# Performance work log

Hardware: AMD Instinct MI355X
Metric: run time of the kernel (lower is better)

## Reference

```python
import jax, jax.numpy as jnp
import numpy as np

S = 32   # parent grid side
G = 64   # child grid side (2*S)
C = 16   # channels
DN = ('NDHWC', 'DHWIO', 'NDHWC')


def conv3(t, w, b):
    # t: [D,H,W,Cin] dense grid; zero padding == nonexistent coords contribute 0 (ME semantics)
    return jax.lax.conv_general_dilated(t[None], w, (1, 1, 1), 'SAME', dimension_numbers=DN)[0] + b


def _grids():
    ix = jnp.arange(G)
    px = (ix % 2)[:, None, None]
    py = (ix % 2)[None, :, None]
    pz = (ix % 2)[None, None, :]
    oct_m = {(a, b, c): (px == a) & (py == b) & (pz == c)
             for a in (0, 1) for b in (0, 1) for c in (0, 1)}
    groups6 = [[(0, 0, 0)], [(1, 1, 0)], [(1, 0, 1)], [(0, 1, 1)],
               [(1, 0, 0), (0, 1, 0)], [(0, 0, 1), (1, 1, 1)]]
    g6 = [jnp.any(jnp.stack([oct_m[o] for o in g]), 0) for g in groups6]
    s3 = (ix // 2)[:, None, None] + (ix // 2)[None, :, None] + (ix // 2)[None, None, :]
    m3 = [(s3 % 3) == j for j in range(3)]  # 3-way repartition (group_mask_gen_par)
    return g6, m3


def coder(feat, occ, w1, b1, w2, b2):
    # ProbCoder: conv -> ReLU -> conv -> sigmoid; outputs exist only at input coords
    of = occ[..., None].astype(feat.dtype)
    h = jax.nn.relu(conv3(feat, w1, b1)) * of
    return jax.nn.sigmoid(conv3(h, w2, b2)) * of


def union(a, b):
    (fa, oa), (fb, ob) = a, b
    return (jnp.where(oa[..., None], fa, fb), oa | ob)


def _forward(x, w_down, b_down, w_fel1, b_fel1, w_fel2, b_fel2, w_up, b_up,
             wc1, bc1, wc2, bc2, wl1, bl1, wl2, bl2):
    g6, m3 = _grids()
    occ_x = x[..., 0] > 0                                    # GT occupied child voxels
    # down (stride-2 conv): coordinate effect only -- last_POV uses ones_like features
    p_occ = jnp.any(occ_x.reshape(S, 2, S, 2, S, 2), axis=(1, 3, 5))  # parent coords
    pf = p_occ[..., None].astype(x.dtype)                    # last_POV features (ones)
    # FEL (dfa): conv(1->C,k3)+ReLU+conv(C->C,k3), outputs only at existing parents
    h = jax.nn.relu(conv3(pf, w_fel1, b_fel1)) * pf
    h = conv3(h, w_fel2, b_fel2) * pf                        # [S,S,S,C]
    # generative transposed conv k2 s2: each parent emits 8 children (octant-specific weight)
    up = jnp.einsum('xyzc,ocd->xyzod', h, w_up) + b_up       # [S,S,S,8,C]
    up = up.reshape(S, S, S, 2, 2, 2, C).transpose(0, 3, 1, 4, 2, 5, 6).reshape(G, G, G, C)
    occ = jnp.repeat(jnp.repeat(jnp.repeat(p_occ, 2, 0), 2, 1), 2, 2)  # child coords of prob
    prob_f = up * occ[..., None]
    lab = [occ_x & g for g in g6]                            # generate_label: GT per group
    # ---------- anchor1 compression (3 sub-stages inside octant group 1) ----------
    a1_o = occ & g6[0]
    a1_f = prob_f * a1_o[..., None]
    r = [(a1_f * m[..., None], a1_o & m) for m in m3]
    lab1 = [lab[0] & m for m in m3]
    p11 = coder(r[0][0], r[0][1], wc1[0], bc1[0], wc2[0], bc2[0])
    d1s = (prob_f * lab1[0][..., None], lab1[0])             # decoded GT of sub-stage 1
    in2 = union(r[1], d1s)
    p12 = coder(in2[0], in2[1], wl1[0], bl1[0], wl2[0], bl2[0]) * (in2[1] & m3[1])[..., None]
    d2s = (prob_f * lab1[1][..., None], lab1[1])
    in3 = union(union(d1s, d2s), r[2])
    p13 = coder(in3[0], in3[1], wl1[1], bl1[1], wl2[1], bl2[1]) * (in3[1] & m3[2])[..., None]
    # ---------- anchors 2..6 ----------
    dec = (prob_f * lab[0][..., None], lab[0])               # prob_anchor1_dec
    probs = [p11, p12, p13]
    for k in range(1, 6):
        ak_o = occ & g6[k]
        ak = (prob_f * ak_o[..., None], ak_o)
        inp = union(dec, ak)
        pk = coder(inp[0], inp[1], wc1[k], bc1[k], wc2[k], bc2[k]) * (inp[1] & g6[k])[..., None]
        probs.append(pk)
        if k < 5:
            dk = (prob_f * lab[k][..., None], lab[k])
            dec = union(dec, dk)
    probs = jnp.stack([p[..., 0] for p in probs], 0)          # [8,G,G,G]
    labels = jnp.stack([lab1[0], lab1[1], lab1[2], lab[1], lab[2], lab[3], lab[4], lab[5]], 0).astype(x.dtype)
    return probs, labels


def setup_inputs() -> dict:
    key = jax.random.key(0)
    ks = jax.random.split(key, 20)
    f = lambda k, s: jax.random.normal(k, s, jnp.float32) * 0.1
    x = (jax.random.uniform(ks[0], (G, G, G, 1)) < 0.5).astype(jnp.float32)
    return {
        'x': x,
        'w_down': f(ks[1], (2, 2, 2, 1, 1)), 'b_down': f(ks[2], (1,)),
        'w_fel1': f(ks[3], (3, 3, 3, 1, C)), 'b_fel1': f(ks[4], (C,)),
        'w_fel2': f(ks[5], (3, 3, 3, C, C)), 'b_fel2': f(ks[6], (C,)),
        'w_up': f(ks[7], (8, C, C)), 'b_up': f(ks[8], (C,)),
        'wc1': f(ks[9], (6, 3, 3, 3, C, C)), 'bc1': f(ks[10], (6, C)),
        'wc2': f(ks[11], (6, 3, 3, 3, C, 1)), 'bc2': f(ks[12], (6, 1)),
        'wl1': f(ks[13], (2, 5, 5, 5, C, C)), 'bl1': f(ks[14], (2, C)),
        'wl2': f(ks[15], (2, 5, 5, 5, C, 1)), 'bl2': f(ks[16], (2, 1)),
    }


def reference(x, w_down, b_down, w_fel1, b_fel1, w_fel2, b_fel2, w_up, b_up,
              wc1, bc1, wc2, bc2, wl1, bl1, wl2, bl2):
    return _forward(x, w_down, b_down, w_fel1, b_fel1, w_fel2, b_fel2, w_up, b_up,
                    wc1, bc1, wc2, bc2, wl1, bl1, wl2, bl2)
```

## Files before the change

kernel.cpp:

```cpp
#include <hip/hip_runtime.h>
#include <cstdint>
#include <math.h>

#define G 64
#define S 32
#define G3 (G*G*G)
#define S3 (S*S*S)

typedef unsigned long long u64;
typedef unsigned int u32;
typedef unsigned short u16;

typedef __attribute__((ext_vector_type(8))) short s16x8;
typedef __attribute__((ext_vector_type(4))) float f32x4;

__device__ __forceinline__ float sigmoidf_(float v) {
    return 1.0f / (1.0f + expf(-v));
}
__device__ __forceinline__ u32 f2bf_rne(float f) {
    u32 u = __float_as_uint(f);
    u += 0x7fff + ((u >> 16) & 1);
    return u >> 16;
}
__device__ __forceinline__ u64 rfl64(u64 v) {
    u32 lo = __builtin_amdgcn_readfirstlane((u32)v);
    u32 hi = __builtin_amdgcn_readfirstlane((u32)(v >> 32));
    return ((u64)hi << 32) | lo;
}
__device__ __forceinline__ u64 tap_hit(u64 wout, u64 wn, int dz) {
    return (dz >= 0) ? (wout & (wn >> dz)) : (wout & (wn << (-dz)));
}
__device__ __forceinline__ void gload16(const void* g, void* l) {
    __builtin_amdgcn_global_load_lds(
        (const __attribute__((address_space(1))) unsigned int*)g,
        (__attribute__((address_space(3))) unsigned int*)l, 16, 0, 0);
}

__global__ __launch_bounds__(256) void k_pocc(const float* __restrict__ x,
                                              unsigned char* __restrict__ pocc) {
    int p = blockIdx.x * 256 + threadIdx.x;
    if (p >= S3) return;
    int pz = p & 31, py = (p >> 5) & 31, px = p >> 10;
    const float* b = x + (((size_t)(px * 2) * G + py * 2) * G + pz * 2);
    bool occ = false;
    #pragma unroll
    for (int a = 0; a < 2; a++)
        #pragma unroll
        for (int bb = 0; bb < 2; bb++)
            #pragma unroll
            for (int c = 0; c < 2; c++)
                occ = occ || (b[((size_t)a * G + bb) * G + c] > 0.0f);
    pocc[p] = occ ? 1 : 0;
}

__global__ __launch_bounds__(256) void k_fel1(const unsigned char* __restrict__ pocc,
                                              const float* __restrict__ w1,
                                              const float* __restrict__ b1,
                                              float* __restrict__ h1) {
    int idx = blockIdx.x * 256 + threadIdx.x;
    int p = idx >> 4, co = idx & 15;
    int pz = p & 31, py = (p >> 5) & 31, px = p >> 10;
    if (!pocc[p]) { h1[idx] = 0.0f; return; }
    float a = b1[co];
    for (int dx = -1; dx <= 1; ++dx) {
        int nx = px + dx; if ((unsigned)nx >= S) continue;
        for (int dy = -1; dy <= 1; ++dy) {
            int ny = py + dy; if ((unsigned)ny >= S) continue;
            for (int dz = -1; dz <= 1; ++dz) {
                int nz = pz + dz; if ((unsigned)nz >= S) continue;
                if (pocc[(nx * S + ny) * S + nz])
                    a += w1[(((dx + 1) * 3 + (dy + 1)) * 3 + (dz + 1)) * 16 + co];
            }
        }
    }
    h1[idx] = fmaxf(a, 0.0f);
}

__global__ __launch_bounds__(256) void k_fel2(const unsigned char* __restrict__ pocc,
                                              const float* __restrict__ h1,
                                              const float* __restrict__ w2,
                                              const float* __restrict__ b2,
                                              float* __restrict__ h2) {
    int idx = blockIdx.x * 256 + threadIdx.x;
    int p = idx >> 4, co = idx & 15;
    int pz = p & 31, py = (p >> 5) & 31, px = p >> 10;
    if (!pocc[p]) { h2[idx] = 0.0f; return; }
    float a = b2[co];
    for (int dx = -1; dx <= 1; ++dx) {
        int nx = px + dx; if ((unsigned)nx >= S) continue;
        for (int dy = -1; dy <= 1; ++dy) {
            int ny = py + dy; if ((unsigned)ny >= S) continue;
            for (int dz = -1; dz <= 1; ++dz) {
                int nz = pz + dz; if ((unsigned)nz >= S) continue;
                const float* f = h1 + (size_t)((nx * S + ny) * S + nz) * 16;
                const float* ww = w2 + (size_t)(((dx + 1) * 3 + (dy + 1)) * 3 + (dz + 1)) * 256 + co;
                #pragma unroll
                for (int ci = 0; ci < 16; ++ci)
                    a = fmaf(f[ci], ww[ci * 16], a);
            }
        }
    }
    h2[idx] = a;
}

__global__ __launch_bounds__(256) void k_up(const unsigned char* __restrict__ pocc,
                                            const float* __restrict__ h2,
                                            const float* __restrict__ wup,
                                            const float* __restrict__ bup,
                                            u16* __restrict__ pf) {
    int idx = blockIdx.x * 256 + threadIdx.x;
    int p = idx >> 3, o = idx & 7;
    int pz = p & 31, py = (p >> 5) & 31, px = p >> 10;
    bool occ = pocc[p] != 0;
    int a = o >> 2, b = (o >> 1) & 1, c = o & 1;
    int line = (2 * px + a) * G + (2 * py + b);
    u16* op = pf + ((size_t)line * 64 + (2 * pz + c)) * 16;
    uint4* o4 = reinterpret_cast<uint4*>(op);
    if (!occ) {
        o4[0] = make_uint4(0, 0, 0, 0);
        o4[1] = make_uint4(0, 0, 0, 0);
        return;
    }
    float h[16];
    const float* hp = h2 + (size_t)p * 16;
    #pragma unroll
    for (int i = 0; i < 16; i++) h[i] = hp[i];
    u32 pk[8];
    #pragma unroll
    for (int i = 0; i < 8; ++i) {
        float a0 = bup[2 * i], a1 = bup[2 * i + 1];
        #pragma unroll
        for (int cc = 0; cc < 16; cc++) {
            a0 = fmaf(h[cc], wup[(o * 16 + cc) * 16 + 2 * i], a0);
            a1 = fmaf(h[cc], wup[(o * 16 + cc) * 16 + 2 * i + 1], a1);
        }
        pk[i] = f2bf_rne(a0) | (f2bf_rne(a1) << 16);
    }
    o4[0] = make_uint4(pk[0], pk[1], pk[2], pk[3]);
    o4[1] = make_uint4(pk[4], pk[5], pk[6], pk[7]);
}

__global__ __launch_bounds__(256) void k_masks(const float* __restrict__ x,
                                               const unsigned char* __restrict__ pocc,
                                               u64* __restrict__ lw_in,
                                               u64* __restrict__ lw_fin,
                                               unsigned char* __restrict__ m_in,
                                               float* __restrict__ labels) {
    int z = threadIdx.x;
    int y = blockIdx.x * 4 + threadIdx.y;
    int xx = blockIdx.y;
    int v = (xx * G + y) * G + z;
    int par = ((xx & 1) << 2) | ((y & 1) << 1) | (z & 1);
    const int gmap[8] = {0, 5, 4, 3, 4, 2, 1, 5};
    int g = gmap[par];
    int t = ((xx >> 1) + (y >> 1) + (z >> 1)) % 3;
    bool occ = pocc[(((xx >> 1) * S) + (y >> 1)) * S + (z >> 1)] != 0;
    bool ox = x[v] > 0.0f;
    bool g0 = (g == 0);

    bool mi[8], mf[8], lb[8];
    mi[0] = occ && g0 && (t == 0);
    mi[1] = (occ && g0 && (t == 1)) || (ox && g0 && (t == 0));
    mi[2] = (ox && g0 && (t < 2)) || (occ && g0 && (t == 2));
    mi[3] = (ox && g0)       || (occ && (g == 1));
    mi[4] = (ox && (g <= 1)) || (occ && (g == 2));
    mi[5] = (ox && (g <= 2)) || (occ && (g == 3));
    mi[6] = (ox && (g <= 3)) || (occ && (g == 4));
    mi[7] = (ox && (g <= 4)) || (occ && (g == 5));

    mf[0] = occ && g0 && (t == 0);
    mf[1] = occ && g0 && (t == 1);
    mf[2] = occ && g0 && (t == 2);
    mf[3] = occ && (g == 1);
    mf[4] = occ && (g == 2);
    mf[5] = occ && (g == 3);
    mf[6] = occ && (g == 4);
    mf[7] = occ && (g == 5);

    lb[0] = ox && g0 && (t == 0);
    lb[1] = ox && g0 && (t == 1);
    lb[2] = ox && g0 && (t == 2);
    lb[3] = ox && (g == 1);
    lb[4] = ox && (g == 2);
    lb[5] = ox && (g == 3);
    lb[6] = ox && (g == 4);
    lb[7] = ox && (g == 5);

    int line = xx * G + y;
    u32 mbyte = 0;
    #pragma unroll
    for (int c = 0; c < 8; ++c) {
        u64 wi = __ballot((int)mi[c]);
        u64 wf = __ballot((int)mf[c]);
        if (z == 0) {
            lw_in[c * 4096 + line] = wi;
            lw_fin[c * 4096 + line] = wf;
        }
        mbyte |= ((u32)mi[c]) << c;
        labels[(size_t)c * G3 + v] = lb[c] ? 1.0f : 0.0f;
    }
    m_in[v] = (unsigned char)mbyte;
}

__global__ __launch_bounds__(256) void k_maskprob(const u16* __restrict__ pf,
                                                  const unsigned char* __restrict__ m_in,
                                                  u16* __restrict__ mprob,
                                                  int b0, int nb) {
    int gid = blockIdx.x * 256 + threadIdx.x;
    size_t off = (size_t)gid * 8;
    uint4 d = *reinterpret_cast<const uint4*>(pf + off);
    unsigned char mb = m_in[gid >> 1];
    const uint4 z = make_uint4(0, 0, 0, 0);
    for (int ci = 0; ci < nb; ++ci) {
        int c = b0 + ci;
        uint4 o = ((mb >> c) & 1) ? d : z;
        *reinterpret_cast<uint4*>(mprob + (size_t)ci * G3 * 16 + off) = o;
    }
}

#define FRAGSTRIDE 38400
__global__ __launch_bounds__(64) void k_prep_bfrag(const float* __restrict__ wc1,
                                                   const float* __restrict__ wl1,
                                                   u16* __restrict__ bfrag) {
    int c = blockIdx.x;
    int frag = blockIdx.y;
    int lane = threadIdx.x;
    bool is5 = (c == 1 || c == 2);
    int R = is5 ? 2 : 1;
    int KS = 2 * R + 1;
    int npair = R + 1;
    int nfrag = KS * KS * npair;
    if (frag >= nfrag) return;
    const float* W = is5 ? (wl1 + (size_t)(c - 1) * 32000)
                         : (wc1 + (size_t)((c == 0) ? 0 : (c - 2)) * 6912);
    int dxdy = frag / npair, p = frag - dxdy * npair;
    int dziA = 2 * p;
    int co = lane & 15, kg = lane >> 4;
    u16 outv[8];
    #pragma unroll
    for (int j = 0; j < 8; ++j) {
        int k = kg * 8 + j;
        int ci = k & 15;
        int dzi = (k < 16) ? dziA : (dziA + 1);
        float v = 0.0f;
        if (dzi < KS)
            v = W[(size_t)(dxdy * KS + dzi) * 256 + ci * 16 + co];
        outv[j] = (u16)f2bf_rne(v);
    }
    u16* o = bfrag + (size_t)c * FRAGSTRIDE + ((size_t)frag * 64 + lane) * 8;
    uint4 pk;
    pk.x = outv[0] | ((u32)outv[1] << 16);
    pk.y = outv[2] | ((u32)outv[3] << 16);
    pk.z = outv[4] | ((u32)outv[5] << 16);
    pk.w = outv[6] | ((u32)outv[7] << 16);
    *reinterpret_cast<uint4*>(o) = pk;
}

__global__ __launch_bounds__(256) void k_conv1_mfma(const u16* __restrict__ mprob,
                                                    const u64* __restrict__ lw_in,
                                                    const u16* __restrict__ bfrag,
                                                    const float* __restrict__ bc1,
                                                    const float* __restrict__ bl1,
                                                    u16* __restrict__ hbase,
                                                    int b0) {
    int ci = blockIdx.y;
    int c = b0 + ci;
    bool is5 = (c == 1 || c == 2);
    int R = is5 ? 2 : 1;
    int KS = 2 * R + 1, npair = R + 1;
    const u64* lw = lw_in + (size_t)c * 4096;
    u16* h_c = hbase + (size_t)ci * G3 * 16;
    const u16* mp = mprob + (size_t)ci * G3 * 16;
    const u16* bf = bfrag + (size_t)c * FRAGSTRIDE;
    const float* bptr = is5 ? (bl1 + (c - 1) * 16)
                            : (bc1 + ((c == 0) ? 0 : (c - 2)) * 16);

    int x = blockIdx.x >> 4;
    int y0 = (blockIdx.x & 15) << 2;
    int w = threadIdx.y;
    int lane = threadIdx.x;
    int yw = y0 + w;

    u64 w0 = rfl64(lw[x * G + yw]);
    u64 anyw = lw[x * G + y0] | lw[x * G + y0 + 1] | lw[x * G + y0 + 2] | lw[x * G + y0 + 3];
    if (anyw == 0ULL) return;

    __shared__ u32 lds[8 * 2304 / 4];
    char* ldsc = reinterpret_cast<char*>(lds);

    int col = lane & 15, kg = lane >> 4;
    float bv = bptr[col];
    f32x4 acc[4];
    #pragma unroll
    for (int s = 0; s < 4; ++s) acc[s] = (f32x4){bv, bv, bv, bv};

    int t = w * 64 + lane;
    if (t < 128) {
        int slot = t >> 4, q = t & 15;
        int off = (q < 8) ? (q * 16) : (2176 + (q - 8) * 16);
        *reinterpret_cast<uint4*>(ldsc + slot * 2304 + off) = make_uint4(0, 0, 0, 0);
    }

    u32 goff = ((u32)lane >> 1) * 32 +
               ((((u32)lane & 1) ^ (((u32)lane >> 3) & 1) ^ 1u) * 16);

    int nlines = 4 + 2 * R;

    for (int dx = -R; dx <= R; ++dx) {
        int nx = x + dx;
        __syncthreads();
        if ((unsigned)nx < G) {
            for (int s = w; s < nlines; s += 4) {
                int ny = y0 - R + s;
                if ((unsigned)ny >= G) continue;
                if (lw[nx * G + ny] == 0ULL) continue;
                const char* src = reinterpret_cast<const char*>(mp + (size_t)(nx * G + ny) * 1024) + goff;
                char* dst = ldsc + s * 2304 + 128;
                gload16(src, dst);
                gload16(src + 1024, dst + 1024);
            }
        }
        __syncthreads();
        if (w0 == 0ULL || (unsigned)nx >= G) continue;

        for (int dy = -R; dy <= R; ++dy) {
            int ny = yw + dy;
            if ((unsigned)ny >= G) continue;
            u64 wn = rfl64(lw[nx * G + ny]);
            if (wn == 0ULL) continue;
            int slot = w + dy + R;
            for (int p = 0; p < npair; ++p) {
                int dzA = -R + 2 * p;
                int dzB = dzA + 1;
                bool hasB = (dzB <= R);
                u64 hit = tap_hit(w0, wn, dzA);
                if (hasB) hit |= tap_hit(w0, wn, dzB);
                if (hit == 0ULL) continue;
                int frag = ((dx + R) * KS + (dy + R)) * npair + p;
                s16x8 bf8 = *reinterpret_cast<const s16x8*>(bf + ((size_t)frag * 64 + lane) * 8);
                int dz = (kg < 2) ? dzA : (hasB ? dzB : dzA);
                int lzb = col + dz + 4;
                const char* ab = ldsc + slot * 2304 + lzb * 32
                                 + (((kg & 1) ^ ((lzb >> 2) & 1)) * 16);
                #pragma unroll
                for (int s = 0; s < 4; ++s) {
                    if (((hit >> (s * 16)) & 0xFFFFULL) == 0ULL) continue;
                    s16x8 a = *reinterpret_cast<const s16x8*>(ab + s * 512);
                    acc[s] = __builtin_amdgcn_mfma_f32_16x16x32_bf16(a, bf8, acc[s], 0, 0, 0);
                }
            }
        }
    }

    if (w0 == 0ULL) return;
    u16* hline = h_c + (size_t)(x * G + yw) * G * 16;
    #pragma unroll
    for (int s = 0; s < 4; ++s) {
        #pragma unroll
        for (int r = 0; r < 4; ++r) {
            int z = s * 16 + kg * 4 + r;
            if ((w0 >> z) & 1) {
                float v = fmaxf(acc[s][r], 0.0f);
                hline[z * 16 + col] = (u16)f2bf_rne(v);
            }
        }
    }
}

template <int KS>
__device__ __forceinline__ void conv2_body(const u32* __restrict__ h_c,
                                           const u64* __restrict__ lwi,
                                           const u64* __restrict__ lwf,
                                           const float* __restrict__ w2,
                                           const float* __restrict__ b2,
                                           float* __restrict__ outp) {
    const int R = KS / 2;
    int z = threadIdx.x;
    int line = blockIdx.x * 4 + threadIdx.y;
    int xx = line >> 6, y = line & 63;
    int v = (xx * G + y) * G + z;
    u64 wf = rfl64(lwf[line]);
    if (wf == 0ULL) { outp[v] = 0.0f; return; }
    bool m = (wf >> z) & 1;

    float ac0 = 0.0f, ac1 = 0.0f;
    for (int dx = -R; dx <= R; ++dx) {
        int nx = xx + dx; if ((unsigned)nx >= G) continue;
        for (int dy = -R; dy <= R; ++dy) {
            int ny = y + dy; if ((unsigned)ny >= G) continue;
            u64 wn = rfl64(lwi[nx * G + ny]);
            if (wn == 0ULL) continue;
            const float* wbase = w2 + (size_t)(((dx + R) * KS + (dy + R)) * KS) * 16;
            #pragma unroll
            for (int dz = -R; dz <= R; ++dz) {
                if (tap_hit(wf, wn, dz) == 0ULL) continue;
                int nz = z + dz;
                bool ok = (unsigned)nz < G;
                int nzc = ok ? nz : 0;
                bool mn = ok && ((wn >> nzc) & 1);
                const float* w = wbase + (dz + R) * 16;
                if (mn) {
                    const uint4* h4 = reinterpret_cast<const uint4*>(
                        h_c + ((size_t)((nx * G + ny) * G + nzc)) * 8);
                    uint4 Ua = h4[0], Ub = h4[1];
                    u32 uu[8] = {Ua.x, Ua.y, Ua.z, Ua.w, Ub.x, Ub.y, Ub.z, Ub.w};
                    float s0 = 0.0f, s1 = 0.0f;
                    #pragma unroll
                    for (int i = 0; i < 8; ++i) {
                        float lo = __uint_as_float(uu[i] << 16);
                        float hi = __uint_as_float(uu[i] & 0xffff0000u);
                        s0 = fmaf(lo, w[2 * i], s0);
                        s1 = fmaf(hi, w[2 * i + 1], s1);
                    }
                    if (((dz + R) & 1) == 0) ac0 += s0 + s1;
                    else                     ac1 += s0 + s1;
                }
            }
        }
    }
    float acc = b2[0] + ac0 + ac1;
    outp[v] = m ? sigmoidf_(acc) : 0.0f;
}

__global__ __launch_bounds__(256) void k_conv2_all(const u32* __restrict__ hbase,
                                                   const u64* __restrict__ lw_in,
                                                   const u64* __restrict__ lw_fin,
                                                   const float* __restrict__ wc2,
                                                   const float* __restrict__ bc2,
                                                   const float* __restrict__ wl2,
                                                   const float* __restrict__ bl2,
                                                   float* __restrict__ out,
                                                   int b0) {
    int ci = blockIdx.y;
    int c = b0 + ci;
    const u64* lwi = lw_in + (size_t)c * 4096;
    const u64* lwf = lw_fin + (size_t)c * 4096;
    const u32* h_c = hbase + (size_t)ci * G3 * 8;
    float* outp = out + (size_t)c * G3;
    if (c == 1 || c == 2) {
        conv2_body<5>(h_c, lwi, lwf, wl2 + (size_t)(c - 1) * 2000, bl2 + (c - 1), outp);
    } else {
        int j = (c == 0) ? 0 : (c - 2);
        conv2_body<3>(h_c, lwi, lwf, wc2 + (size_t)j * 432, bc2 + j, outp);
    }
}

extern "C" void kernel_launch(void* const* d_in, const int* in_sizes, int n_in,
                              void* d_out, int out_size, void* d_ws, size_t ws_size,
                              hipStream_t stream) {
    const float* x      = (const float*)d_in[0];
    const float* w_fel1 = (const float*)d_in[3];
    const float* b_fel1 = (const float*)d_in[4];
    const float* w_fel2 = (const float*)d_in[5];
    const float* b_fel2 = (const float*)d_in[6];
    const float* w_up   = (const float*)d_in[7];
    const float* b_up   = (const float*)d_in[8];
    const float* wc1    = (const float*)d_in[9];
    const float* bc1    = (const float*)d_in[10];
    const float* wc2    = (const float*)d_in[11];
    const float* bc2    = (const float*)d_in[12];
    const float* wl1    = (const float*)d_in[13];
    const float* bl1    = (const float*)d_in[14];
    const float* wl2    = (const float*)d_in[15];
    const float* bl2    = (const float*)d_in[16];
    float* out = (float*)d_out;

    char* ws = (char*)d_ws;
    u16*  probf16 = (u16*)(ws);
    float* h1     = (float*)(ws + 8388608);
    float* h2     = (float*)(ws + 10485760);
    unsigned char* pocc = (unsigned char*)(ws + 12582912);
    u64* lw_in  = (u64*)(ws + 12615680);
    u64* lw_fin = (u64*)(ws + 12877824);
    u16* bfrag  = (u16*)(ws + 13139968);
    unsigned char* m_in = (unsigned char*)(ws + 8388608);
    u16* mprob  = (u16*)(ws + 13754368);

    int NB = 4;
    if (13754368 + (size_t)16 * 8388608 <= ws_size) NB = 8;
    u16* hbase = (u16*)(ws + 13754368 + (size_t)NB * 8388608);

    k_pocc <<<dim3(S3 / 256), dim3(256), 0, stream>>>(x, pocc);
    k_fel1 <<<dim3(S3 * 16 / 256), dim3(256), 0, stream>>>(pocc, w_fel1, b_fel1, h1);
    k_fel2 <<<dim3(S3 * 16 / 256), dim3(256), 0, stream>>>(pocc, h1, w_fel2, b_fel2, h2);
    k_up   <<<dim3(S3 * 8 / 256), dim3(256), 0, stream>>>(pocc, h2, w_up, b_up, probf16);
    k_masks<<<dim3(16, 64), dim3(64, 4), 0, stream>>>(x, pocc, lw_in, lw_fin, m_in,
                                                      out + (size_t)8 * G3);
    k_prep_bfrag<<<dim3(8, 75), dim3(64), 0, stream>>>(wc1, wl1, bfrag);

    for (int b0 = 0; b0 < 8; b0 += NB) {
        int nb = (8 - b0 < NB) ? (8 - b0) : NB;
        k_maskprob<<<dim3(G3 * 16 / 8 / 256), dim3(256), 0, stream>>>(probf16, m_in, mprob, b0, nb);
        k_conv1_mfma<<<dim3(1024, nb), dim3(64, 4), 0, stream>>>(
            mprob, lw_in, bfrag, bc1, bl1, hbase, b0);
        k_conv2_all<<<dim3(1024, nb), dim3(64, 4), 0, stream>>>(
            (const u32*)hbase, lw_in, lw_fin, wc2, bc2, wl2, bl2, out, b0);
    }
}
```

Before: 210.9 us.

## Fuse per-coder input masking into conv1 LDS staging, drop masked-prob buffers

Removes the k_maskprob pass, which wrote eight masked copies of the 16-channel bf16 probability grid. conv1 now loads the shared unmasked grid into LDS and zeroes the rows of inactive voxels using the per-line occupancy bitmask. Without the masked buffers all eight coders fit in the workspace, so conv1 and conv2 each run once over all coders instead of in batches. In exchange conv1 waits on its loads before doing the extra masking stores, which adds a little latency to each dx step.

```diff
diff --git a/kernel.cpp b/kernel.cpp
--- a/kernel.cpp
+++ b/kernel.cpp
@@ -144,7 +144,6 @@
                                                const unsigned char* __restrict__ pocc,
                                                u64* __restrict__ lw_in,
                                                u64* __restrict__ lw_fin,
-                                               unsigned char* __restrict__ m_in,
                                                float* __restrict__ labels) {
     int z = threadIdx.x;
     int y = blockIdx.x * 4 + threadIdx.y;
@@ -187,7 +186,6 @@
     lb[7] = ox && (g == 5);
 
     int line = xx * G + y;
-    u32 mbyte = 0;
     #pragma unroll
     for (int c = 0; c < 8; ++c) {
         u64 wi = __ballot((int)mi[c]);
@@ -196,25 +194,7 @@
             lw_in[c * 4096 + line] = wi;
             lw_fin[c * 4096 + line] = wf;
         }
-        mbyte |= ((u32)mi[c]) << c;
         labels[(size_t)c * G3 + v] = lb[c] ? 1.0f : 0.0f;
-    }
-    m_in[v] = (unsigned char)mbyte;
-}
-
-__global__ __launch_bounds__(256) void k_maskprob(const u16* __restrict__ pf,
-                                                  const unsigned char* __restrict__ m_in,
-                                                  u16* __restrict__ mprob,
-                                                  int b0, int nb) {
-    int gid = blockIdx.x * 256 + threadIdx.x;
-    size_t off = (size_t)gid * 8;
-    uint4 d = *reinterpret_cast<const uint4*>(pf + off);
-    unsigned char mb = m_in[gid >> 1];
-    const uint4 z = make_uint4(0, 0, 0, 0);
-    for (int ci = 0; ci < nb; ++ci) {
-        int c = b0 + ci;
-        uint4 o = ((mb >> c) & 1) ? d : z;
-        *reinterpret_cast<uint4*>(mprob + (size_t)ci * G3 * 16 + off) = o;
     }
 }
 
@@ -256,21 +236,18 @@
     *reinterpret_cast<uint4*>(o) = pk;
 }
 
-__global__ __launch_bounds__(256) void k_conv1_mfma(const u16* __restrict__ mprob,
+__global__ __launch_bounds__(256) void k_conv1_mfma(const u16* __restrict__ pf,
                                                     const u64* __restrict__ lw_in,
                                                     const u16* __restrict__ bfrag,
                                                     const float* __restrict__ bc1,
                                                     const float* __restrict__ bl1,
-                                                    u16* __restrict__ hbase,
-                                                    int b0) {
-    int ci = blockIdx.y;
-    int c = b0 + ci;
+                                                    u16* __restrict__ hbase) {
+    int c = blockIdx.y;
     bool is5 = (c == 1 || c == 2);
     int R = is5 ? 2 : 1;
     int KS = 2 * R + 1, npair = R + 1;
     const u64* lw = lw_in + (size_t)c * 4096;
-    u16* h_c = hbase + (size_t)ci * G3 * 16;
-    const u16* mp = mprob + (size_t)ci * G3 * 16;
+    u16* h_c = hbase + (size_t)c * G3 * 16;
     const u16* bf = bfrag + (size_t)c * FRAGSTRIDE;
     const float* bptr = is5 ? (bl1 + (c - 1) * 16)
                             : (bc1 + ((c == 0) ? 0 : (c - 2)) * 16);
@@ -312,12 +289,25 @@
         if ((unsigned)nx < G) {
             for (int s = w; s < nlines; s += 4) {
                 int ny = y0 - R + s;
-                if ((unsigned)ny >= G) continue;
-                if (lw[nx * G + ny] == 0ULL) continue;
-                const char* src = reinterpret_cast<const char*>(mp + (size_t)(nx * G + ny) * 1024) + goff;
-                char* dst = ldsc + s * 2304 + 128;
-                gload16(src, dst);
-                gload16(src + 1024, dst + 1024);
+                u64 wn = ((unsigned)ny < G) ? lw[nx * G + ny] : 0ULL;
+                if (wn != 0ULL) {
+                    const char* src = reinterpret_cast<const char*>(
+                        pf + (size_t)(nx * G + ny) * 1024) + goff;
+                    char* dst = ldsc + s * 2304 + 128;
+                    gload16(src, dst);
+                    gload16(src + 1024, dst + 1024);
+                }
+            }
+            asm volatile("s_waitcnt vmcnt(0)" ::: "memory");
+            for (int s = w; s < nlines; s += 4) {
+                int ny = y0 - R + s;
+                u64 wn = ((unsigned)ny < G) ? lw[nx * G + ny] : 0ULL;
+                bool live = (wn >> lane) & 1;
+                if (!live) {
+                    char* d = ldsc + s * 2304 + (lane + 4) * 32;
+                    *reinterpret_cast<uint4*>(d) = make_uint4(0, 0, 0, 0);
+                    *reinterpret_cast<uint4*>(d + 16) = make_uint4(0, 0, 0, 0);
+                }
             }
         }
         __syncthreads();
@@ -429,13 +419,11 @@
                                                    const float* __restrict__ bc2,
                                                    const float* __restrict__ wl2,
                                                    const float* __restrict__ bl2,
-                                                   float* __restrict__ out,
-                                                   int b0) {
-    int ci = blockIdx.y;
-    int c = b0 + ci;
+                                                   float* __restrict__ out) {
+    int c = blockIdx.y;
     const u64* lwi = lw_in + (size_t)c * 4096;
     const u64* lwf = lw_fin + (size_t)c * 4096;
-    const u32* h_c = hbase + (size_t)ci * G3 * 8;
+    const u32* h_c = hbase + (size_t)c * G3 * 8;
     float* outp = out + (size_t)c * G3;
     if (c == 1 || c == 2) {
         conv2_body<5>(h_c, lwi, lwf, wl2 + (size_t)(c - 1) * 2000, bl2 + (c - 1), outp);
@@ -473,27 +461,17 @@
     u64* lw_in  = (u64*)(ws + 12615680);
     u64* lw_fin = (u64*)(ws + 12877824);
     u16* bfrag  = (u16*)(ws + 13139968);
-    unsigned char* m_in = (unsigned char*)(ws + 8388608);
-    u16* mprob  = (u16*)(ws + 13754368);
-
-    int NB = 4;
-    if (13754368 + (size_t)16 * 8388608 <= ws_size) NB = 8;
-    u16* hbase = (u16*)(ws + 13754368 + (size_t)NB * 8388608);
+    u16* hbase  = (u16*)(ws + 13754368);
 
     k_pocc <<<dim3(S3 / 256), dim3(256), 0, stream>>>(x, pocc);
     k_fel1 <<<dim3(S3 * 16 / 256), dim3(256), 0, stream>>>(pocc, w_fel1, b_fel1, h1);
     k_fel2 <<<dim3(S3 * 16 / 256), dim3(256), 0, stream>>>(pocc, h1, w_fel2, b_fel2, h2);
     k_up   <<<dim3(S3 * 8 / 256), dim3(256), 0, stream>>>(pocc, h2, w_up, b_up, probf16);
-    k_masks<<<dim3(16, 64), dim3(64, 4), 0, stream>>>(x, pocc, lw_in, lw_fin, m_in,
-                                                      out + (size_t)8 * G3);
+    k_masks<<<dim3(16, 64), dim3(64, 4), 0, stream>>>(x, pocc, lw_in, lw_fin, out + (size_t)8 * G3);
     k_prep_bfrag<<<dim3(8, 75), dim3(64), 0, stream>>>(wc1, wl1, bfrag);
 
-    for (int b0 = 0; b0 < 8; b0 += NB) {
-        int nb = (8 - b0 < NB) ? (8 - b0) : NB;
-        k_maskprob<<<dim3(G3 * 16 / 8 / 256), dim3(256), 0, stream>>>(probf16, m_in, mprob, b0, nb);
-        k_conv1_mfma<<<dim3(1024, nb), dim3(64, 4), 0, stream>>>(
-            mprob, lw_in, bfrag, bc1, bl1, hbase, b0);
-        k_conv2_all<<<dim3(1024, nb), dim3(64, 4), 0, stream>>>(
-            (const u32*)hbase, lw_in, lw_fin, wc2, bc2, wl2, bl2, out, b0);
-    }
-}
+    k_conv1_mfma<<<dim3(1024, 8), dim3(64, 4), 0, stream>>>(
+        probf16, lw_in, bfrag, bc1, bl1, hbase);
+    k_conv2_all<<<dim3(1024, 8), dim3(64, 4), 0, stream>>>(
+        (const u32*)hbase, lw_in, lw_fin, wc2, bc2, wl2, bl2, out);
+}
```

Result: no change. 209.9 us (median of 2 runs) (-0.5%).
